# Performance work log

Measured on AMD Instinct MI355X. Metric: run time of the kernel, lower is better.

Reference implementation:

```python
import jax, jax.numpy as jnp
import numpy as np

N_NODES = 50000
N_EDGES = 800000
DIM = 128


def setup_inputs() -> dict:
    key = jax.random.key(0)
    k1, k2, k3, k4, k5 = jax.random.split(key, 5)
    X = jax.random.normal(k1, (N_NODES, DIM), dtype=jnp.float32)
    src = jax.random.randint(k2, (N_EDGES,), 0, N_NODES, dtype=jnp.int64)
    dst = jax.random.randint(k3, (N_EDGES,), 0, N_NODES, dtype=jnp.int64)
    W_self = jax.random.normal(k4, (DIM, DIM), dtype=jnp.float32) * (1.0 / np.sqrt(DIM))
    W_neigh = jax.random.normal(k5, (DIM, DIM), dtype=jnp.float32) * (1.0 / np.sqrt(DIM))
    bias = jnp.zeros((DIM,), dtype=jnp.float32)
    return {"X": X, "src": src, "dst": dst, "W_self": W_self, "W_neigh": W_neigh, "bias": bias}


def reference(X, src, dst, W_self, W_neigh, bias):
    # h[u] = ReLU(W_self x_u + sum_{v in N(u)} W_neigh x_v + b)
    # Transform once per node, then gather per edge and segment-sum into dst.
    h_self = X @ W_self.T                       # [N, out]
    xw = X @ W_neigh.T                          # [N, out]
    h_neigh = jax.ops.segment_sum(xw[src], dst, num_segments=N_NODES)  # [N, out]
    return jax.nn.relu(h_self + h_neigh + bias)
```

## Files before the change

### kernel.cpp

```cpp
#include <hip/hip_runtime.h>
#include <hip/hip_bf16.h>

#define NN 50000
#define NE 800000
#define DIM 128
#define NBLK 49

#define NBUCK 196
#define CAP   6144
#define EPB   3125

typedef __attribute__((ext_vector_type(8))) short bf16x8;
typedef __attribute__((ext_vector_type(4))) float f32x4;

__device__ __forceinline__ short f2bf(float f) {
    union { float f; unsigned u; } x; x.f = f;
    unsigned r = x.u + 0x7fffu + ((x.u >> 16) & 1u);
    return (short)(r >> 16);
}

__device__ __forceinline__ bf16x8 pack8(float4 a, float4 b) {
    bf16x8 v;
    v[0] = f2bf(a.x); v[1] = f2bf(a.y); v[2] = f2bf(a.z); v[3] = f2bf(a.w);
    v[4] = f2bf(b.x); v[5] = f2bf(b.y); v[6] = f2bf(b.z); v[7] = f2bf(b.w);
    return v;
}

__device__ __forceinline__ float bf2f(short s) {
    union { unsigned u; float f; } x; x.u = ((unsigned)(unsigned short)s) << 16;
    return x.f;
}


__global__ __launch_bounds__(256) void part1(const float* __restrict__ X,
                                             const int* __restrict__ src,
                                             const int* __restrict__ dst,
                                             short* __restrict__ Xb,
                                             int* __restrict__ bucketFill,
                                             unsigned* __restrict__ edges) {
    __shared__ unsigned stage[EPB];
    __shared__ unsigned sorted_[EPB];
    __shared__ int lcnt[256];
    __shared__ int lst[256];
    __shared__ int goff[256];
    __shared__ int c2[256];

    int b = blockIdx.x;
    int t = threadIdx.x;

    if (b < 3125) {
        int i = b * 256 + t;
        const float4* p = (const float4*)(X + (size_t)i * 8);
        *(bf16x8*)(Xb + (size_t)i * 8) = pack8(p[0], p[1]);
        return;
    }

    int pb = b - 3125;
    int e0 = pb * EPB;
    lcnt[t] = 0; c2[t] = 0;
    __syncthreads();

    for (int i = t; i < EPB; i += 256) {
        int s = src[e0 + i];
        int d = dst[e0 + i];
        unsigned bk = (unsigned)d >> 8;
        unsigned dl = (unsigned)d & 255u;
        stage[i] = (bk << 24) | (dl << 16) | (unsigned)s;
        atomicAdd(&lcnt[bk], 1);
    }
    __syncthreads();

    int v = lcnt[t];
    for (int off = 1; off < 256; off <<= 1) {
        __syncthreads();
        int tmp = (t >= off) ? lcnt[t - off] : 0;
        __syncthreads();
        lcnt[t] += tmp;
    }
    __syncthreads();
    int excl = lcnt[t] - v;
    lst[t] = excl;
    if (t < NBUCK) {
        int gb = atomicAdd(&bucketFill[t], v);
        goff[t] = t * CAP + gb - excl;
    }
    __syncthreads();

    for (int i = t; i < EPB; i += 256) {
        unsigned p = stage[i];
        int j = p >> 24;
        int r = atomicAdd(&c2[j], 1);
        sorted_[lst[j] + r] = p;
    }
    __syncthreads();

    for (int i = t; i < EPB; i += 256) {
        unsigned p = sorted_[i];
        int j = p >> 24;
        edges[(size_t)goff[j] + i] = p;
    }
}

__global__ __launch_bounds__(256) void pull2(const short* __restrict__ Xb,
                                             const int* __restrict__ bucketFill,
                                             const unsigned* __restrict__ edges,
                                             short* __restrict__ aggb) {
    __shared__ int cnt[32];
    __shared__ int c2s[32];
    __shared__ int start[33];
    __shared__ unsigned short lcsr[1024];

    int t = threadIdx.x;
    int b  = blockIdx.x >> 3;
    int sl = blockIdx.x & 7;
    int dlo = sl * 32;
    int m = bucketFill[b];
    const unsigned* ed = edges + (size_t)b * CAP;

    if (t < 32) { cnt[t] = 0; c2s[t] = 0; }
    __syncthreads();

    for (int i = t; i < m; i += 256) {
        int o = ((ed[i] >> 16) & 255u) - dlo;
        if ((unsigned)o < 32u) atomicAdd(&cnt[o], 1);
    }
    __syncthreads();

    int v = (t < 32) ? cnt[t] : 0;
    for (int off = 1; off < 32; off <<= 1) {
        __syncthreads();
        int tmp = (t >= off && t < 32) ? cnt[t - off] : 0;
        __syncthreads();
        if (t < 32) cnt[t] += tmp;
    }
    __syncthreads();
    if (t < 32) start[t] = cnt[t] - v;
    if (t == 31) start[32] = cnt[31];
    __syncthreads();

    for (int i = t; i < m; i += 256) {
        unsigned p = ed[i];
        int o = ((p >> 16) & 255u) - dlo;
        if ((unsigned)o < 32u) {
            int r = atomicAdd(&c2s[o], 1);
            lcsr[start[o] + r] = (unsigned short)(p & 0xffffu);
        }
    }
    __syncthreads();

    int lane = t & 63, wv = t >> 6;
    int g = lane >> 4, fl = lane & 15;
    const short* xbase = Xb + fl * 8;
    for (int n = wv; n < 32; n += 4) {
        int u = (b << 8) + dlo + n;
        if (u >= NN) continue;
        int beg = start[n], end = start[n + 1];
        f32x4 aA = {0.f, 0.f, 0.f, 0.f}, aB = {0.f, 0.f, 0.f, 0.f};
        int e = beg;
        for (; e + 8 <= end; e += 8) {
            int v0 = lcsr[e + g];
            int v1 = lcsr[e + 4 + g];
            bf16x8 x0 = *(const bf16x8*)(xbase + (size_t)v0 * DIM);
            bf16x8 x1 = *(const bf16x8*)(xbase + (size_t)v1 * DIM);
            aA[0] += bf2f(x0[0]); aA[1] += bf2f(x0[1]); aA[2] += bf2f(x0[2]); aA[3] += bf2f(x0[3]);
            aB[0] += bf2f(x0[4]); aB[1] += bf2f(x0[5]); aB[2] += bf2f(x0[6]); aB[3] += bf2f(x0[7]);
            aA[0] += bf2f(x1[0]); aA[1] += bf2f(x1[1]); aA[2] += bf2f(x1[2]); aA[3] += bf2f(x1[3]);
            aB[0] += bf2f(x1[4]); aB[1] += bf2f(x1[5]); aB[2] += bf2f(x1[6]); aB[3] += bf2f(x1[7]);
        }
        for (; e < end; e += 4) {
            int idx = e + g;
            int vv = lcsr[idx < end ? idx : beg];
            bf16x8 x = *(const bf16x8*)(xbase + (size_t)vv * DIM);
            if (idx < end) {
                aA[0] += bf2f(x[0]); aA[1] += bf2f(x[1]); aA[2] += bf2f(x[2]); aA[3] += bf2f(x[3]);
                aB[0] += bf2f(x[4]); aB[1] += bf2f(x[5]); aB[2] += bf2f(x[6]); aB[3] += bf2f(x[7]);
            }
        }
        #pragma unroll
        for (int i = 0; i < 4; ++i) {
            aA[i] += __shfl_xor(aA[i], 16); aA[i] += __shfl_xor(aA[i], 32);
            aB[i] += __shfl_xor(aB[i], 16); aB[i] += __shfl_xor(aB[i], 32);
        }
        if (g == 0) {
            bf16x8 r;
            r[0] = f2bf(aA[0]); r[1] = f2bf(aA[1]); r[2] = f2bf(aA[2]); r[3] = f2bf(aA[3]);
            r[4] = f2bf(aB[0]); r[5] = f2bf(aB[1]); r[6] = f2bf(aB[2]); r[7] = f2bf(aB[3]);
            *(bf16x8*)(aggb + (size_t)u * DIM + fl * 8) = r;
        }
    }
}

__global__ __launch_bounds__(256) void gemm_bb(const short* __restrict__ Xb,
                                               const short* __restrict__ aggb,
                                               const float* __restrict__ Ws,
                                               const float* __restrict__ Wn,
                                               const float* __restrict__ bias,
                                               float* __restrict__ out) {
    __shared__ __align__(16) short wlds[2][128][128];
    for (int i = threadIdx.x; i < 128 * 16; i += 256) {
        int row = i >> 4;
        int c8 = (i & 15) << 3;
        int sc = c8 ^ ((row & 15) << 3);
        const float4* ps = (const float4*)(Ws + row * DIM + c8);
        *(bf16x8*)&wlds[0][row][sc] = pack8(ps[0], ps[1]);
        const float4* pn = (const float4*)(Wn + row * DIM + c8);
        *(bf16x8*)&wlds[1][row][sc] = pack8(pn[0], pn[1]);
    }
    __syncthreads();

    int lane = threadIdx.x & 63;
    int wv = threadIdx.x >> 6;
    int n0 = blockIdx.x * 64 + wv * 16;
    int arow = n0 + (lane & 15);
    int rowc = arow < NN ? arow : (NN - 1);
    const short* xr = Xb   + (size_t)rowc * DIM + (lane >> 4) * 8;
    const short* ar = aggb + (size_t)rowc * DIM + (lane >> 4) * 8;

    f32x4 acc[8] = {};
    #pragma unroll
    for (int ks = 0; ks < 4; ++ks) {
        int k0 = ks * 32;
        bf16x8 afx = *(const bf16x8*)(xr + k0);
        bf16x8 afg = *(const bf16x8*)(ar + k0);
        int bcol = k0 + (lane >> 4) * 8;
        #pragma unroll
        for (int ot = 0; ot < 8; ++ot) {
            int brow = ot * 16 + (lane & 15);
            int sc = bcol ^ ((brow & 15) << 3);
            bf16x8 bs = *(const bf16x8*)&wlds[0][brow][sc];
            bf16x8 bn = *(const bf16x8*)&wlds[1][brow][sc];
            acc[ot] = __builtin_amdgcn_mfma_f32_16x16x32_bf16(afx, bs, acc[ot], 0, 0, 0);
            acc[ot] = __builtin_amdgcn_mfma_f32_16x16x32_bf16(afg, bn, acc[ot], 0, 0, 0);
        }
    }

    int col0 = lane & 15;
    int rbase = n0 + (lane >> 4) * 4;
    #pragma unroll
    for (int ot = 0; ot < 8; ++ot) {
        int col = ot * 16 + col0;
        float bv = bias[col];
        #pragma unroll
        for (int i = 0; i < 4; ++i) {
            int r = rbase + i;
            if (r < NN) out[(size_t)r * DIM + col] = fmaxf(acc[ot][i] + bv, 0.f);
        }
    }
}


__global__ __launch_bounds__(256) void hist_k(const int* __restrict__ dst,
                                              int* __restrict__ cnt) {
    int e = blockIdx.x * 256 + threadIdx.x;
    if (e < NE) atomicAdd(&cnt[dst[e]], 1);
}

__global__ __launch_bounds__(1024) void scanA(const int* __restrict__ cnt,
                                              int* __restrict__ rowstart,
                                              int* __restrict__ bsum) {
    __shared__ int s[1024];
    int i = blockIdx.x * 1024 + threadIdx.x;
    int v = (i < NN) ? cnt[i] : 0;
    s[threadIdx.x] = v;
    for (int off = 1; off < 1024; off <<= 1) {
        __syncthreads();
        int t = (threadIdx.x >= off) ? s[threadIdx.x - off] : 0;
        __syncthreads();
        s[threadIdx.x] += t;
    }
    __syncthreads();
    if (i < NN) rowstart[i] = s[threadIdx.x] - v;
    if (threadIdx.x == 1023) bsum[blockIdx.x] = s[1023];
}

__global__ __launch_bounds__(64) void scanB(int* __restrict__ bsum) {
    int l = threadIdx.x;
    int orig = (l < NBLK) ? bsum[l] : 0;
    int v = orig;
    for (int off = 1; off < 64; off <<= 1) {
        int t = __shfl_up(v, off);
        if (l >= off) v += t;
    }
    if (l < NBLK) bsum[l] = v - orig;
}

__global__ __launch_bounds__(1024) void scanC(int* __restrict__ rowstart,
                                              const int* __restrict__ bsum) {
    int i = blockIdx.x * 1024 + threadIdx.x;
    if (i < NN) rowstart[i] += bsum[blockIdx.x];
    if (i == 0) rowstart[NN] = NE;
}

__global__ __launch_bounds__(256) void fill_atomic(const int* __restrict__ src,
                                                   const int* __restrict__ dst,
                                                   int* __restrict__ rowstart,
                                                   int* __restrict__ csr) {
    int e = blockIdx.x * 256 + threadIdx.x;
    if (e < NE) {
        int p = atomicAdd(&rowstart[dst[e]], 1);
        csr[p] = src[e];
    }
}

__global__ __launch_bounds__(256) void cvt_k(const float* __restrict__ X,
                                             short* __restrict__ Xb) {
    int i = blockIdx.x * 256 + threadIdx.x;
    if (i < NN * DIM / 8) {
        const float4* p = (const float4*)(X + (size_t)i * 8);
        *(bf16x8*)(Xb + (size_t)i * 8) = pack8(p[0], p[1]);
    }
}

__global__ __launch_bounds__(256) void pull_bf16(const short* __restrict__ Xb,
                                                 const int* __restrict__ rowend,
                                                 const int* __restrict__ csr,
                                                 float* __restrict__ agg) {
    int lane = threadIdx.x & 63;
    int u = (blockIdx.x * 256 + threadIdx.x) >> 6;
    if (u >= NN) return;
    int beg = (u == 0) ? 0 : rowend[u - 1];
    int end = rowend[u];
    float2 a0 = {0.f, 0.f}, a1 = {0.f, 0.f};
    int e = beg;
    for (; e + 1 < end; e += 2) {
        int v0 = csr[e], v1 = csr[e + 1];
        ushort2 x0 = *(const ushort2*)(Xb + (size_t)v0 * DIM + lane * 2);
        ushort2 x1 = *(const ushort2*)(Xb + (size_t)v1 * DIM + lane * 2);
        a0.x += bf2f(x0.x); a0.y += bf2f(x0.y);
        a1.x += bf2f(x1.x); a1.y += bf2f(x1.y);
    }
    if (e < end) {
        int v0 = csr[e];
        ushort2 x0 = *(const ushort2*)(Xb + (size_t)v0 * DIM + lane * 2);
        a0.x += bf2f(x0.x); a0.y += bf2f(x0.y);
    }
    float2 r = {a0.x + a1.x, a0.y + a1.y};
    *(float2*)(agg + (size_t)u * DIM + lane * 2) = r;
}

__global__ __launch_bounds__(256) void scatter_k(const float* __restrict__ X,
                                                 const int* __restrict__ src,
                                                 const int* __restrict__ dst,
                                                 float* __restrict__ agg) {
    int lane = threadIdx.x & 63;
    int gw = (blockIdx.x * 256 + threadIdx.x) >> 6;
    int nw = (gridDim.x * 256) >> 6;
    for (int e = gw; e < NE; e += nw) {
        int s = src[e];
        int d = dst[e];
        float2 v = *(const float2*)(X + (size_t)s * DIM + lane * 2);
        float* a = agg + (size_t)d * DIM + lane * 2;
        unsafeAtomicAdd(a, v.x);
        unsafeAtomicAdd(a + 1, v.y);
    }
}

__global__ __launch_bounds__(256) void fused_gemm(
        const float* __restrict__ X,
        const float* __restrict__ agg,
        const float* __restrict__ Ws,
        const float* __restrict__ Wn,
        const float* __restrict__ bias,
        float* __restrict__ out) {
    __shared__ __align__(16) short wlds[2][128][128];
    for (int i = threadIdx.x; i < 128 * 16; i += 256) {
        int row = i >> 4;
        int c8 = (i & 15) << 3;
        int sc = c8 ^ ((row & 15) << 3);
        const float4* ps = (const float4*)(Ws + row * DIM + c8);
        *(bf16x8*)&wlds[0][row][sc] = pack8(ps[0], ps[1]);
        const float4* pn = (const float4*)(Wn + row * DIM + c8);
        *(bf16x8*)&wlds[1][row][sc] = pack8(pn[0], pn[1]);
    }
    __syncthreads();

    int lane = threadIdx.x & 63;
    int wv = threadIdx.x >> 6;
    int n0 = blockIdx.x * 64 + wv * 16;
    int arow = n0 + (lane & 15);
    int rowc = arow < NN ? arow : (NN - 1);
    const float* xr = X + (size_t)rowc * DIM + (lane >> 4) * 8;
    const float* ar = agg + (size_t)rowc * DIM + (lane >> 4) * 8;

    f32x4 acc[8] = {};
    #pragma unroll
    for (int ks = 0; ks < 4; ++ks) {
        int k0 = ks * 32;
        float4 xa = *(const float4*)(xr + k0);
        float4 xb = *(const float4*)(xr + k0 + 4);
        bf16x8 afx = pack8(xa, xb);
        float4 ga = *(const float4*)(ar + k0);
        float4 gb = *(const float4*)(ar + k0 + 4);
        bf16x8 afg = pack8(ga, gb);
        int bcol = k0 + (lane >> 4) * 8;
        #pragma unroll
        for (int ot = 0; ot < 8; ++ot) {
            int brow = ot * 16 + (lane & 15);
            int sc = bcol ^ ((brow & 15) << 3);
            bf16x8 bs = *(const bf16x8*)&wlds[0][brow][sc];
            bf16x8 bn = *(const bf16x8*)&wlds[1][brow][sc];
            acc[ot] = __builtin_amdgcn_mfma_f32_16x16x32_bf16(afx, bs, acc[ot], 0, 0, 0);
            acc[ot] = __builtin_amdgcn_mfma_f32_16x16x32_bf16(afg, bn, acc[ot], 0, 0, 0);
        }
    }

    int col0 = lane & 15;
    int rbase = n0 + (lane >> 4) * 4;
    #pragma unroll
    for (int ot = 0; ot < 8; ++ot) {
        int col = ot * 16 + col0;
        float bv = bias[col];
        #pragma unroll
        for (int i = 0; i < 4; ++i) {
            int r = rbase + i;
            if (r < NN) out[(size_t)r * DIM + col] = fmaxf(acc[ot][i] + bv, 0.f);
        }
    }
}


extern "C" void kernel_launch(void* const* d_in, const int* in_sizes, int n_in,
                              void* d_out, int out_size, void* d_ws, size_t ws_size,
                              hipStream_t stream) {
    const float* X    = (const float*)d_in[0];
    const int*   src  = (const int*)  d_in[1];
    const int*   dst  = (const int*)  d_in[2];
    const float* Ws   = (const float*)d_in[3];
    const float* Wn   = (const float*)d_in[4];
    const float* bias = (const float*)d_in[5];
    float* out = (float*)d_out;

    const size_t REQ0 = ((size_t)256 + (size_t)NBUCK * CAP
                      + (size_t)NN * DIM / 2 * 2) * 4;
    const size_t REQ2 = (size_t)(50048 + 50056 + 64 + 800000) * 4
                      + (size_t)NN * DIM * 2;

    if (ws_size >= REQ0) {
        int*      bf    = (int*)d_ws;
        unsigned* edges = (unsigned*)(bf + 256);
        short*    Xb    = (short*)(edges + (size_t)NBUCK * CAP);
        short*    aggb  = Xb + (size_t)NN * DIM;

        hipMemsetAsync(bf, 0, 256 * sizeof(int), stream);
        part1<<<3125 + 256, 256, 0, stream>>>(X, src, dst, Xb, bf, edges);
        pull2<<<NBUCK * 8, 256, 0, stream>>>(Xb, bf, edges, aggb);
        gemm_bb<<<(NN + 63) / 64, 256, 0, stream>>>(Xb, aggb, Ws, Wn, bias, out);
    } else if (ws_size >= REQ2) {
        int* cnt      = (int*)d_ws;
        int* rowstart = cnt + 50048;
        int* bsum     = rowstart + 50056;
        int* csr      = bsum + 64;
        short* Xb     = (short*)(csr + 800000);

        hipMemsetAsync(cnt, 0, 50048 * sizeof(int), stream);
        hist_k<<<3125, 256, 0, stream>>>(dst, cnt);
        scanA<<<NBLK, 1024, 0, stream>>>(cnt, rowstart, bsum);
        scanB<<<1, 64, 0, stream>>>(bsum);
        scanC<<<NBLK, 1024, 0, stream>>>(rowstart, bsum);
        fill_atomic<<<3125, 256, 0, stream>>>(src, dst, rowstart, csr);
        cvt_k<<<3125, 256, 0, stream>>>(X, Xb);
        pull_bf16<<<12500, 256, 0, stream>>>(Xb, rowstart, csr, out);
        fused_gemm<<<(NN + 63) / 64, 256, 0, stream>>>(X, out, Ws, Wn, bias, out);
    } else {
        hipMemsetAsync(out, 0, (size_t)NN * DIM * sizeof(float), stream);
        scatter_k<<<2048, 256, 0, stream>>>(X, src, dst, out);
        fused_gemm<<<(NN + 63) / 64, 256, 0, stream>>>(X, out, Ws, Wn, bias, out);
    }
}
```

Before: 87.34 us.

## Vectorize edge partition loads, deepen gather unroll, enlarge GEMM blocks, replace memset

The edge partition and bucket scans now read src/dst/edge words as int4/uint4 vectors with 3200 edges per block over 250 blocks. The neighbor gather gains a 16-edge unrolled path so more loads are in flight at once. The GEMM runs 512-thread blocks covering 128 rows each, so the LDS weight staging is amortized over twice as many rows. The memset is replaced by a tiny zeroing kernel to cut API overhead. The unaligned tail in pull2 uses a scalar fallback, and the larger GEMM blocks may lower occupancy.

```diff
diff --git a/kernel.cpp b/kernel.cpp
--- a/kernel.cpp
+++ b/kernel.cpp
@@ -8,7 +8,8 @@
 
 #define NBUCK 196
 #define CAP   6144
-#define EPB   3125
+#define EPB   3200
+#define PBLK  250
 
 typedef __attribute__((ext_vector_type(8))) short bf16x8;
 typedef __attribute__((ext_vector_type(4))) float f32x4;
@@ -29,6 +30,15 @@
 __device__ __forceinline__ float bf2f(short s) {
     union { unsigned u; float f; } x; x.u = ((unsigned)(unsigned short)s) << 16;
     return x.f;
+}
+
+__device__ __forceinline__ void acc8(f32x4& aA, f32x4& aB, bf16x8 x) {
+    aA[0] += bf2f(x[0]); aA[1] += bf2f(x[1]); aA[2] += bf2f(x[2]); aA[3] += bf2f(x[3]);
+    aB[0] += bf2f(x[4]); aB[1] += bf2f(x[5]); aB[2] += bf2f(x[6]); aB[3] += bf2f(x[7]);
+}
+
+__global__ __launch_bounds__(256) void zero_k(int* __restrict__ p) {
+    p[threadIdx.x] = 0;
 }
 
 
@@ -60,13 +70,18 @@
     lcnt[t] = 0; c2[t] = 0;
     __syncthreads();
 
-    for (int i = t; i < EPB; i += 256) {
-        int s = src[e0 + i];
-        int d = dst[e0 + i];
-        unsigned bk = (unsigned)d >> 8;
-        unsigned dl = (unsigned)d & 255u;
-        stage[i] = (bk << 24) | (dl << 16) | (unsigned)s;
-        atomicAdd(&lcnt[bk], 1);
+    for (int i = t * 4; i < EPB; i += 1024) {
+        int4 s4 = *(const int4*)(src + e0 + i);
+        int4 d4 = *(const int4*)(dst + e0 + i);
+        int ss[4] = {s4.x, s4.y, s4.z, s4.w};
+        int dd[4] = {d4.x, d4.y, d4.z, d4.w};
+        #pragma unroll
+        for (int j = 0; j < 4; ++j) {
+            unsigned bk = (unsigned)dd[j] >> 8;
+            unsigned dl = (unsigned)dd[j] & 255u;
+            stage[i + j] = (bk << 24) | (dl << 16) | (unsigned)ss[j];
+            atomicAdd(&lcnt[bk], 1);
+        }
     }
     __syncthreads();
 
@@ -86,18 +101,26 @@
     }
     __syncthreads();
 
-    for (int i = t; i < EPB; i += 256) {
-        unsigned p = stage[i];
-        int j = p >> 24;
-        int r = atomicAdd(&c2[j], 1);
-        sorted_[lst[j] + r] = p;
-    }
-    __syncthreads();
-
-    for (int i = t; i < EPB; i += 256) {
-        unsigned p = sorted_[i];
-        int j = p >> 24;
-        edges[(size_t)goff[j] + i] = p;
+    for (int i = t * 4; i < EPB; i += 1024) {
+        uint4 p4 = *(const uint4*)&stage[i];
+        unsigned pp[4] = {p4.x, p4.y, p4.z, p4.w};
+        #pragma unroll
+        for (int j = 0; j < 4; ++j) {
+            int bj = pp[j] >> 24;
+            int r = atomicAdd(&c2[bj], 1);
+            sorted_[lst[bj] + r] = pp[j];
+        }
+    }
+    __syncthreads();
+
+    for (int i = t * 4; i < EPB; i += 1024) {
+        uint4 p4 = *(const uint4*)&sorted_[i];
+        unsigned pp[4] = {p4.x, p4.y, p4.z, p4.w};
+        #pragma unroll
+        for (int j = 0; j < 4; ++j) {
+            int bj = pp[j] >> 24;
+            edges[(size_t)goff[bj] + i + j] = pp[j];
+        }
     }
 }
 
@@ -120,9 +143,21 @@
     if (t < 32) { cnt[t] = 0; c2s[t] = 0; }
     __syncthreads();
 
-    for (int i = t; i < m; i += 256) {
-        int o = ((ed[i] >> 16) & 255u) - dlo;
-        if ((unsigned)o < 32u) atomicAdd(&cnt[o], 1);
+    for (int i = t * 4; i < m; i += 1024) {
+        if (i + 4 <= m) {
+            uint4 e4 = *(const uint4*)(ed + i);
+            unsigned pp[4] = {e4.x, e4.y, e4.z, e4.w};
+            #pragma unroll
+            for (int j = 0; j < 4; ++j) {
+                int o = ((pp[j] >> 16) & 255u) - dlo;
+                if ((unsigned)o < 32u) atomicAdd(&cnt[o], 1);
+            }
+        } else {
+            for (int k = i; k < m; ++k) {
+                int o = ((ed[k] >> 16) & 255u) - dlo;
+                if ((unsigned)o < 32u) atomicAdd(&cnt[o], 1);
+            }
+        }
     }
     __syncthreads();
 
@@ -138,12 +173,27 @@
     if (t == 31) start[32] = cnt[31];
     __syncthreads();
 
-    for (int i = t; i < m; i += 256) {
-        unsigned p = ed[i];
-        int o = ((p >> 16) & 255u) - dlo;
-        if ((unsigned)o < 32u) {
-            int r = atomicAdd(&c2s[o], 1);
-            lcsr[start[o] + r] = (unsigned short)(p & 0xffffu);
+    for (int i = t * 4; i < m; i += 1024) {
+        if (i + 4 <= m) {
+            uint4 e4 = *(const uint4*)(ed + i);
+            unsigned pp[4] = {e4.x, e4.y, e4.z, e4.w};
+            #pragma unroll
+            for (int j = 0; j < 4; ++j) {
+                int o = ((pp[j] >> 16) & 255u) - dlo;
+                if ((unsigned)o < 32u) {
+                    int r = atomicAdd(&c2s[o], 1);
+                    lcsr[start[o] + r] = (unsigned short)(pp[j] & 0xffffu);
+                }
+            }
+        } else {
+            for (int k = i; k < m; ++k) {
+                unsigned p = ed[k];
+                int o = ((p >> 16) & 255u) - dlo;
+                if ((unsigned)o < 32u) {
+                    int r = atomicAdd(&c2s[o], 1);
+                    lcsr[start[o] + r] = (unsigned short)(p & 0xffffu);
+                }
+            }
         }
     }
     __syncthreads();
@@ -157,24 +207,30 @@
         int beg = start[n], end = start[n + 1];
         f32x4 aA = {0.f, 0.f, 0.f, 0.f}, aB = {0.f, 0.f, 0.f, 0.f};
         int e = beg;
+        for (; e + 16 <= end; e += 16) {
+            int v0 = lcsr[e + g];
+            int v1 = lcsr[e + 4 + g];
+            int v2 = lcsr[e + 8 + g];
+            int v3 = lcsr[e + 12 + g];
+            bf16x8 x0 = *(const bf16x8*)(xbase + (size_t)v0 * DIM);
+            bf16x8 x1 = *(const bf16x8*)(xbase + (size_t)v1 * DIM);
+            bf16x8 x2 = *(const bf16x8*)(xbase + (size_t)v2 * DIM);
+            bf16x8 x3 = *(const bf16x8*)(xbase + (size_t)v3 * DIM);
+            acc8(aA, aB, x0); acc8(aA, aB, x1);
+            acc8(aA, aB, x2); acc8(aA, aB, x3);
+        }
         for (; e + 8 <= end; e += 8) {
             int v0 = lcsr[e + g];
             int v1 = lcsr[e + 4 + g];
             bf16x8 x0 = *(const bf16x8*)(xbase + (size_t)v0 * DIM);
             bf16x8 x1 = *(const bf16x8*)(xbase + (size_t)v1 * DIM);
-            aA[0] += bf2f(x0[0]); aA[1] += bf2f(x0[1]); aA[2] += bf2f(x0[2]); aA[3] += bf2f(x0[3]);
-            aB[0] += bf2f(x0[4]); aB[1] += bf2f(x0[5]); aB[2] += bf2f(x0[6]); aB[3] += bf2f(x0[7]);
-            aA[0] += bf2f(x1[0]); aA[1] += bf2f(x1[1]); aA[2] += bf2f(x1[2]); aA[3] += bf2f(x1[3]);
-            aB[0] += bf2f(x1[4]); aB[1] += bf2f(x1[5]); aB[2] += bf2f(x1[6]); aB[3] += bf2f(x1[7]);
+            acc8(aA, aB, x0); acc8(aA, aB, x1);
         }
         for (; e < end; e += 4) {
             int idx = e + g;
             int vv = lcsr[idx < end ? idx : beg];
             bf16x8 x = *(const bf16x8*)(xbase + (size_t)vv * DIM);
-            if (idx < end) {
-                aA[0] += bf2f(x[0]); aA[1] += bf2f(x[1]); aA[2] += bf2f(x[2]); aA[3] += bf2f(x[3]);
-                aB[0] += bf2f(x[4]); aB[1] += bf2f(x[5]); aB[2] += bf2f(x[6]); aB[3] += bf2f(x[7]);
-            }
+            if (idx < end) acc8(aA, aB, x);
         }
         #pragma unroll
         for (int i = 0; i < 4; ++i) {
@@ -190,14 +246,14 @@
     }
 }
 
-__global__ __launch_bounds__(256) void gemm_bb(const short* __restrict__ Xb,
+__global__ __launch_bounds__(512) void gemm_bb(const short* __restrict__ Xb,
                                                const short* __restrict__ aggb,
                                                const float* __restrict__ Ws,
                                                const float* __restrict__ Wn,
                                                const float* __restrict__ bias,
                                                float* __restrict__ out) {
     __shared__ __align__(16) short wlds[2][128][128];
-    for (int i = threadIdx.x; i < 128 * 16; i += 256) {
+    for (int i = threadIdx.x; i < 128 * 16; i += 512) {
         int row = i >> 4;
         int c8 = (i & 15) << 3;
         int sc = c8 ^ ((row & 15) << 3);
@@ -210,7 +266,7 @@
 
     int lane = threadIdx.x & 63;
     int wv = threadIdx.x >> 6;
-    int n0 = blockIdx.x * 64 + wv * 16;
+    int n0 = blockIdx.x * 128 + wv * 16;
     int arow = n0 + (lane & 15);
     int rowc = arow < NN ? arow : (NN - 1);
     const short* xr = Xb   + (size_t)rowc * DIM + (lane >> 4) * 8;
@@ -441,10 +497,10 @@
         short*    Xb    = (short*)(edges + (size_t)NBUCK * CAP);
         short*    aggb  = Xb + (size_t)NN * DIM;
 
-        hipMemsetAsync(bf, 0, 256 * sizeof(int), stream);
-        part1<<<3125 + 256, 256, 0, stream>>>(X, src, dst, Xb, bf, edges);
+        zero_k<<<1, 256, 0, stream>>>(bf);
+        part1<<<3125 + PBLK, 256, 0, stream>>>(X, src, dst, Xb, bf, edges);
         pull2<<<NBUCK * 8, 256, 0, stream>>>(Xb, bf, edges, aggb);
-        gemm_bb<<<(NN + 63) / 64, 256, 0, stream>>>(Xb, aggb, Ws, Wn, bias, out);
+        gemm_bb<<<(NN + 127) / 128, 512, 0, stream>>>(Xb, aggb, Ws, Wn, bias, out);
     } else if (ws_size >= REQ2) {
         int* cnt      = (int*)d_ws;
         int* rowstart = cnt + 50048;
```

After: 76.09 us. -12.9%, faster.
